# Kernel optimization log

Measured on AMD Instinct MI355X. Metric: run time of the kernel, lower is better.

## Reference

```python
import jax, jax.numpy as jnp
import numpy as np

FACTOR = 5

def setup_inputs() -> dict:
    key = jax.random.key(0)
    kq, kk, kv, ki = jax.random.split(key, 4)
    B, L, H, D = 8, 2048, 8, 64
    u = FACTOR * int(np.ceil(np.log(L)))  # sample_k == n_top == 40
    return {
        "queries": jax.random.normal(kq, (B, L, H, D), dtype=jnp.float32),
        "keys": jax.random.normal(kk, (B, L, H, D), dtype=jnp.float32),
        "values": jax.random.normal(kv, (B, L, H, D), dtype=jnp.float32),
        "index_sample": jax.random.randint(ki, (L, u), 0, L, dtype=jnp.int32),
    }

def reference(queries, keys, values, index_sample):
    B, L, H, D = queries.shape
    # faithful to torch .view(B, H, -1, D) on contiguous tensors (a reshape, not a transpose)
    q = queries.reshape(B, H, L, D)
    k = keys.reshape(B, H, L, D)
    v = values.reshape(B, H, L, D)
    u = FACTOR * int(np.ceil(np.log(L)))  # U_part == u
    # --- _prob_QK: sample keys per query, score, pick top-u queries ---
    K_sample = k[:, :, index_sample, :]                      # [B,H,L,u,D] gather over L_K
    QK_sample = jnp.einsum('bhld,bhlsd->bhls', q, K_sample)  # [B,H,L,u]
    M = QK_sample.max(axis=-1) - QK_sample.sum(axis=-1) / L  # sparsity measure [B,H,L]
    M_top = jax.lax.top_k(M, u)[1]                           # [B,H,u] indices of active queries
    Q_reduce = jnp.take_along_axis(q, M_top[..., None], axis=2)  # [B,H,u,D]
    scores = jnp.einsum('bhud,bhld->bhul', Q_reduce, k)      # [B,H,u,L]
    scale = 1.0 / float(np.sqrt(D))
    attn = jax.nn.softmax(scores * scale, axis=-1)           # dropout is identity in eval
    context = jnp.einsum('bhul,bhld->bhud', attn, v)         # [B,H,u,D]
    return context, attn
```

## Files before the change

kernel.cpp:

```cpp
#include <hip/hip_runtime.h>
#include <math.h>

#define LSEQ 2048
#define DDIM 64
#define UU   40
#define NBH  64
#define CTX_ELEMS (NBH*UU*DDIM)

__global__ __launch_bounds__(256, 4) void k12_sample_m(
    const float* __restrict__ q, const float* __restrict__ k,
    const int* __restrict__ idxs, float* __restrict__ M) {
  int b = blockIdx.x;
  int bh = b & 63;
  int ltile = b >> 6;
  int t = threadIdx.x;
  int g = t >> 2;
  int sub = t & 3;
  int l = ltile * 64 + g;

  const float4* qr = (const float4*)(q + (size_t)(bh * LSEQ + l) * DDIM);
  float4 qv[4];
#pragma unroll
  for (int m = 0; m < 4; ++m) qv[m] = qr[4 * m + sub];

  const float* kbase = k + (size_t)bh * LSEQ * DDIM;
  const int4* ir = (const int4*)(idxs + l * UU);

  float mx = -INFINITY, sm = 0.f;
#pragma unroll 1
  for (int s4 = 0; s4 < UU / 4; ++s4) {
    int4 jv = ir[s4];
    const float4* k0 = (const float4*)(kbase + (size_t)jv.x * DDIM);
    const float4* k1 = (const float4*)(kbase + (size_t)jv.y * DDIM);
    const float4* k2 = (const float4*)(kbase + (size_t)jv.z * DDIM);
    const float4* k3 = (const float4*)(kbase + (size_t)jv.w * DDIM);
    float d0 = 0.f, d1 = 0.f, d2 = 0.f, d3 = 0.f;
#pragma unroll
    for (int m = 0; m < 4; ++m) {
      float4 a = k0[4 * m + sub];
      float4 x = qv[m];
      d0 += x.x * a.x + x.y * a.y + x.z * a.z + x.w * a.w;
    }
#pragma unroll
    for (int m = 0; m < 4; ++m) {
      float4 a = k1[4 * m + sub];
      float4 x = qv[m];
      d1 += x.x * a.x + x.y * a.y + x.z * a.z + x.w * a.w;
    }
#pragma unroll
    for (int m = 0; m < 4; ++m) {
      float4 a = k2[4 * m + sub];
      float4 x = qv[m];
      d2 += x.x * a.x + x.y * a.y + x.z * a.z + x.w * a.w;
    }
#pragma unroll
    for (int m = 0; m < 4; ++m) {
      float4 a = k3[4 * m + sub];
      float4 x = qv[m];
      d3 += x.x * a.x + x.y * a.y + x.z * a.z + x.w * a.w;
    }
    d0 += __shfl_xor(d0, 1, 64); d0 += __shfl_xor(d0, 2, 64);
    d1 += __shfl_xor(d1, 1, 64); d1 += __shfl_xor(d1, 2, 64);
    d2 += __shfl_xor(d2, 1, 64); d2 += __shfl_xor(d2, 2, 64);
    d3 += __shfl_xor(d3, 1, 64); d3 += __shfl_xor(d3, 2, 64);
    mx = fmaxf(fmaxf(fmaxf(mx, d0), fmaxf(d1, d2)), d3);
    sm += (d0 + d1) + (d2 + d3);
  }
  if (sub == 0) M[bh * LSEQ + l] = mx - sm * (1.0f / (float)LSEQ);
}

__global__ __launch_bounds__(256) void k3_topk(const float* __restrict__ M,
                                               int* __restrict__ Mtop) {
  int bh = blockIdx.x;
  int t = threadIdx.x;
  int w = t >> 6;
  int lane = t & 63;
  float v[8];
#pragma unroll
  for (int j = 0; j < 8; ++j) v[j] = M[bh * LSEQ + t + 256 * j];
  __shared__ float swv[4];
  __shared__ int   swi[4];
  __shared__ int   win;
  for (int it = 0; it < UU; ++it) {
    float bv = -INFINITY; int bi = 0x7fffffff;
#pragma unroll
    for (int j = 0; j < 8; ++j) {
      if (v[j] > bv) { bv = v[j]; bi = t + 256 * j; }
    }
#pragma unroll
    for (int off = 32; off > 0; off >>= 1) {
      float ov = __shfl_xor(bv, off, 64);
      int   oi = __shfl_xor(bi, off, 64);
      if (ov > bv || (ov == bv && oi < bi)) { bv = ov; bi = oi; }
    }
    if (lane == 0) { swv[w] = bv; swi[w] = bi; }
    __syncthreads();
    if (t == 0) {
      float fv = swv[0]; int fi = swi[0];
#pragma unroll
      for (int j = 1; j < 4; ++j) {
        if (swv[j] > fv || (swv[j] == fv && swi[j] < fi)) { fv = swv[j]; fi = swi[j]; }
      }
      Mtop[bh * UU + it] = fi;
      win = fi;
    }
    __syncthreads();
    int wi = win;
    if ((wi & 255) == t) v[wi >> 8] = -INFINITY;
  }
}

__global__ __launch_bounds__(256, 4) void k45_scores_softmax(
    const float* __restrict__ q, const float* __restrict__ k,
    const int* __restrict__ Mtop, float* __restrict__ attn,
    float* __restrict__ ctx) {
  __shared__ float sct[4 * LSEQ];
  int b = blockIdx.x;
  int bh = b & 63;
  int u0 = (b >> 6) * 4;
  int t = threadIdx.x;
  int g = t >> 2;
  int sub = t & 3;

  ctx[b * 256 + t] = 0.f;

  float4 qv[4][4];
#pragma unroll
  for (int u = 0; u < 4; ++u) {
    int qi = Mtop[bh * UU + u0 + u];
    const float4* qr = (const float4*)(q + (size_t)(bh * LSEQ + qi) * DDIM);
#pragma unroll
    for (int m = 0; m < 4; ++m) qv[u][m] = qr[4 * m + sub];
  }

  const float* kb = k + (size_t)bh * LSEQ * DDIM;
#pragma unroll 1
  for (int p = 0; p < 32; ++p) {
    int l = p * 64 + g;
    const float4* kr = (const float4*)(kb + (size_t)l * DDIM);
    float4 ks[4];
#pragma unroll
    for (int m = 0; m < 4; ++m) ks[m] = kr[4 * m + sub];
    float d[4];
#pragma unroll
    for (int u = 0; u < 4; ++u) {
      float s = 0.f;
#pragma unroll
      for (int m = 0; m < 4; ++m) {
        float4 x = qv[u][m], a = ks[m];
        s += x.x * a.x + x.y * a.y + x.z * a.z + x.w * a.w;
      }
      s += __shfl_xor(s, 1, 64);
      s += __shfl_xor(s, 2, 64);
      d[u] = s * 0.125f;
    }
    if (sub == 0) {
#pragma unroll
      for (int u = 0; u < 4; ++u) sct[u * LSEQ + l] = d[u];
    }
  }
  __syncthreads();

  int w = t >> 6, lane = t & 63;
  float* row = sct + w * LSEQ;
  float vv[32];
  float mx = -INFINITY;
#pragma unroll
  for (int j = 0; j < 32; ++j) { vv[j] = row[lane + 64 * j]; mx = fmaxf(mx, vv[j]); }
#pragma unroll
  for (int off = 32; off > 0; off >>= 1) mx = fmaxf(mx, __shfl_xor(mx, off, 64));
  float sm = 0.f;
#pragma unroll
  for (int j = 0; j < 32; ++j) { vv[j] = __expf(vv[j] - mx); sm += vv[j]; }
#pragma unroll
  for (int off = 32; off > 0; off >>= 1) sm += __shfl_xor(sm, off, 64);
  float inv = 1.0f / sm;
  float* ap = attn + (size_t)(bh * UU + u0 + w) * LSEQ;
#pragma unroll
  for (int j = 0; j < 32; ++j) ap[lane + 64 * j] = vv[j] * inv;
}

__global__ __launch_bounds__(256) void k7_context(
    const float* __restrict__ attn, const float* __restrict__ v,
    float* __restrict__ ctx) {
  __shared__ float vt[256 * DDIM];
  int b = blockIdx.x;
  int bh = b & 63;
  int l0 = (b >> 6) * 256;
  int t = threadIdx.x;

  const float4* src = (const float4*)(v + ((size_t)bh * LSEQ + l0) * DDIM);
  float4* dst = (float4*)vt;
#pragma unroll
  for (int i = 0; i < 16; ++i) dst[t + 256 * i] = src[t + 256 * i];
  __syncthreads();

  int w = t >> 6;
  int d = t & 63;
  const float* ab = attn + ((size_t)bh * UU + w * 10) * LSEQ + l0;
  float acc[10];
#pragma unroll
  for (int u = 0; u < 10; ++u) acc[u] = 0.f;
#pragma unroll 1
  for (int l4 = 0; l4 < 64; ++l4) {
    int l = l4 * 4;
    float4 av[10];
#pragma unroll
    for (int u = 0; u < 10; ++u)
      av[u] = *(const float4*)(ab + (size_t)u * LSEQ + l);
#pragma unroll
    for (int i = 0; i < 4; ++i) {
      float vvv = vt[(l + i) * DDIM + d];
#pragma unroll
      for (int u = 0; u < 10; ++u)
        acc[u] = fmaf(((const float*)&av[u])[i], vvv, acc[u]);
    }
  }
#pragma unroll
  for (int u = 0; u < 10; ++u)
    atomicAdd(&ctx[((size_t)bh * UU + w * 10 + u) * DDIM + d], acc[u]);
}

extern "C" void kernel_launch(void* const* d_in, const int* in_sizes, int n_in,
                              void* d_out, int out_size, void* d_ws, size_t ws_size,
                              hipStream_t stream) {
  const float* q   = (const float*)d_in[0];
  const float* k   = (const float*)d_in[1];
  const float* v   = (const float*)d_in[2];
  const int*   idx = (const int*)d_in[3];

  float* ctx  = (float*)d_out;
  float* attn = (float*)d_out + CTX_ELEMS;

  float* M    = (float*)d_ws;
  int*   Mtop = (int*)(M + NBH * LSEQ);

  k12_sample_m<<<NBH * 32, 256, 0, stream>>>(q, k, idx, M);
  k3_topk<<<NBH, 256, 0, stream>>>(M, Mtop);
  k45_scores_softmax<<<NBH * 10, 256, 0, stream>>>(q, k, Mtop, attn, ctx);
  k7_context<<<NBH * 8, 256, 0, stream>>>(attn, v, ctx);
}
```

Baseline: 303.9 us.

## Fuse top-k, scores/softmax and context into one kernel per head group

Merges the top-k selection, score/softmax and attention-times-V kernels into a single kernel with 8 blocks per head, each handling 5 selected queries. Every block redundantly recomputes the full 40-step top-k from M so that no Mtop round trip or separate launch is needed. The context product now reads normalized probabilities from shared memory instead of re-reading attn from global, and reduces across warps in shared memory instead of using atomics and a zero-init pass. The cost is 8x redundant top-k work, fewer blocks for the score phase (512 vs 640), and more shared memory per block.

Measured after the change: 327.5 us. +7.8%, slower.

```diff
diff --git a/kernel.cpp b/kernel.cpp
--- a/kernel.cpp
+++ b/kernel.cpp
@@ -37,26 +37,22 @@
     float d0 = 0.f, d1 = 0.f, d2 = 0.f, d3 = 0.f;
 #pragma unroll
     for (int m = 0; m < 4; ++m) {
-      float4 a = k0[4 * m + sub];
-      float4 x = qv[m];
+      float4 a = k0[4 * m + sub]; float4 x = qv[m];
       d0 += x.x * a.x + x.y * a.y + x.z * a.z + x.w * a.w;
     }
 #pragma unroll
     for (int m = 0; m < 4; ++m) {
-      float4 a = k1[4 * m + sub];
-      float4 x = qv[m];
+      float4 a = k1[4 * m + sub]; float4 x = qv[m];
       d1 += x.x * a.x + x.y * a.y + x.z * a.z + x.w * a.w;
     }
 #pragma unroll
     for (int m = 0; m < 4; ++m) {
-      float4 a = k2[4 * m + sub];
-      float4 x = qv[m];
+      float4 a = k2[4 * m + sub]; float4 x = qv[m];
       d2 += x.x * a.x + x.y * a.y + x.z * a.z + x.w * a.w;
     }
 #pragma unroll
     for (int m = 0; m < 4; ++m) {
-      float4 a = k3[4 * m + sub];
-      float4 x = qv[m];
+      float4 a = k3[4 * m + sub]; float4 x = qv[m];
       d3 += x.x * a.x + x.y * a.y + x.z * a.z + x.w * a.w;
     }
     d0 += __shfl_xor(d0, 1, 64); d0 += __shfl_xor(d0, 2, 64);
@@ -69,23 +65,32 @@
   if (sub == 0) M[bh * LSEQ + l] = mx - sm * (1.0f / (float)LSEQ);
 }
 
-__global__ __launch_bounds__(256) void k3_topk(const float* __restrict__ M,
-                                               int* __restrict__ Mtop) {
-  int bh = blockIdx.x;
-  int t = threadIdx.x;
-  int w = t >> 6;
-  int lane = t & 63;
-  float v[8];
-#pragma unroll
-  for (int j = 0; j < 8; ++j) v[j] = M[bh * LSEQ + t + 256 * j];
+__global__ __launch_bounds__(256, 3) void kf_fused(
+    const float* __restrict__ q, const float* __restrict__ k,
+    const float* __restrict__ v, const float* __restrict__ M,
+    float* __restrict__ attn, float* __restrict__ ctx) {
+  __shared__ float sct[5 * LSEQ];
+  __shared__ float red[4 * 5 * 64];
   __shared__ float swv[4];
   __shared__ int   swi[4];
   __shared__ int   win;
+  __shared__ int   topq[5];
+
+  int b = blockIdx.x;
+  int bh = b & 63;
+  int ug = b >> 6;
+  int u0 = ug * 5;
+  int t = threadIdx.x;
+  int w = t >> 6, lane = t & 63;
+
+  float mv[8];
+#pragma unroll
+  for (int j = 0; j < 8; ++j) mv[j] = M[bh * LSEQ + t + 256 * j];
   for (int it = 0; it < UU; ++it) {
     float bv = -INFINITY; int bi = 0x7fffffff;
 #pragma unroll
     for (int j = 0; j < 8; ++j) {
-      if (v[j] > bv) { bv = v[j]; bi = t + 256 * j; }
+      if (mv[j] > bv) { bv = mv[j]; bi = t + 256 * j; }
     }
 #pragma unroll
     for (int off = 32; off > 0; off >>= 1) {
@@ -101,38 +106,24 @@
       for (int j = 1; j < 4; ++j) {
         if (swv[j] > fv || (swv[j] == fv && swi[j] < fi)) { fv = swv[j]; fi = swi[j]; }
       }
-      Mtop[bh * UU + it] = fi;
       win = fi;
+      if (it >= u0 && it < u0 + 5) topq[it - u0] = fi;
     }
     __syncthreads();
     int wi = win;
-    if ((wi & 255) == t) v[wi >> 8] = -INFINITY;
-  }
-}
-
-__global__ __launch_bounds__(256, 4) void k45_scores_softmax(
-    const float* __restrict__ q, const float* __restrict__ k,
-    const int* __restrict__ Mtop, float* __restrict__ attn,
-    float* __restrict__ ctx) {
-  __shared__ float sct[4 * LSEQ];
-  int b = blockIdx.x;
-  int bh = b & 63;
-  int u0 = (b >> 6) * 4;
-  int t = threadIdx.x;
+    if ((wi & 255) == t) mv[wi >> 8] = -INFINITY;
+  }
+
   int g = t >> 2;
   int sub = t & 3;
-
-  ctx[b * 256 + t] = 0.f;
-
-  float4 qv[4][4];
-#pragma unroll
-  for (int u = 0; u < 4; ++u) {
-    int qi = Mtop[bh * UU + u0 + u];
+  float4 qv[5][4];
+#pragma unroll
+  for (int u = 0; u < 5; ++u) {
+    int qi = topq[u];
     const float4* qr = (const float4*)(q + (size_t)(bh * LSEQ + qi) * DDIM);
 #pragma unroll
     for (int m = 0; m < 4; ++m) qv[u][m] = qr[4 * m + sub];
   }
-
   const float* kb = k + (size_t)bh * LSEQ * DDIM;
 #pragma unroll 1
   for (int p = 0; p < 32; ++p) {
@@ -141,9 +132,8 @@
     float4 ks[4];
 #pragma unroll
     for (int m = 0; m < 4; ++m) ks[m] = kr[4 * m + sub];
-    float d[4];
-#pragma unroll
-    for (int u = 0; u < 4; ++u) {
+#pragma unroll
+    for (int u = 0; u < 5; ++u) {
       float s = 0.f;
 #pragma unroll
       for (int m = 0; m < 4; ++m) {
@@ -152,73 +142,68 @@
       }
       s += __shfl_xor(s, 1, 64);
       s += __shfl_xor(s, 2, 64);
-      d[u] = s * 0.125f;
-    }
-    if (sub == 0) {
-#pragma unroll
-      for (int u = 0; u < 4; ++u) sct[u * LSEQ + l] = d[u];
+      if (sub == 0) sct[u * LSEQ + l] = s * 0.125f;
     }
   }
   __syncthreads();
 
-  int w = t >> 6, lane = t & 63;
-  float* row = sct + w * LSEQ;
-  float vv[32];
-  float mx = -INFINITY;
-#pragma unroll
-  for (int j = 0; j < 32; ++j) { vv[j] = row[lane + 64 * j]; mx = fmaxf(mx, vv[j]); }
-#pragma unroll
-  for (int off = 32; off > 0; off >>= 1) mx = fmaxf(mx, __shfl_xor(mx, off, 64));
-  float sm = 0.f;
-#pragma unroll
-  for (int j = 0; j < 32; ++j) { vv[j] = __expf(vv[j] - mx); sm += vv[j]; }
-#pragma unroll
-  for (int off = 32; off > 0; off >>= 1) sm += __shfl_xor(sm, off, 64);
-  float inv = 1.0f / sm;
-  float* ap = attn + (size_t)(bh * UU + u0 + w) * LSEQ;
-#pragma unroll
-  for (int j = 0; j < 32; ++j) ap[lane + 64 * j] = vv[j] * inv;
-}
-
-__global__ __launch_bounds__(256) void k7_context(
-    const float* __restrict__ attn, const float* __restrict__ v,
-    float* __restrict__ ctx) {
-  __shared__ float vt[256 * DDIM];
-  int b = blockIdx.x;
-  int bh = b & 63;
-  int l0 = (b >> 6) * 256;
-  int t = threadIdx.x;
-
-  const float4* src = (const float4*)(v + ((size_t)bh * LSEQ + l0) * DDIM);
-  float4* dst = (float4*)vt;
-#pragma unroll
-  for (int i = 0; i < 16; ++i) dst[t + 256 * i] = src[t + 256 * i];
+  for (int r = w; r < 5; r += 4) {
+    float* row = sct + r * LSEQ;
+    float vv[32];
+    float mx = -INFINITY;
+#pragma unroll
+    for (int j = 0; j < 32; ++j) { vv[j] = row[lane + 64 * j]; mx = fmaxf(mx, vv[j]); }
+#pragma unroll
+    for (int off = 32; off > 0; off >>= 1) mx = fmaxf(mx, __shfl_xor(mx, off, 64));
+    float sm = 0.f;
+#pragma unroll
+    for (int j = 0; j < 32; ++j) { vv[j] = __expf(vv[j] - mx); sm += vv[j]; }
+#pragma unroll
+    for (int off = 32; off > 0; off >>= 1) sm += __shfl_xor(sm, off, 64);
+    float inv = 1.0f / sm;
+    float* ap = attn + (size_t)(bh * UU + u0 + r) * LSEQ;
+#pragma unroll
+    for (int j = 0; j < 32; ++j) {
+      float pn = vv[j] * inv;
+      ap[lane + 64 * j] = pn;
+      row[lane + 64 * j] = pn;
+    }
+  }
   __syncthreads();
 
-  int w = t >> 6;
-  int d = t & 63;
-  const float* ab = attn + ((size_t)bh * UU + w * 10) * LSEQ + l0;
-  float acc[10];
-#pragma unroll
-  for (int u = 0; u < 10; ++u) acc[u] = 0.f;
+  int d = lane;
+  const float* vb = v + (size_t)bh * LSEQ * DDIM;
+  float acc[5] = {0.f, 0.f, 0.f, 0.f, 0.f};
+  int l0 = w * 512;
 #pragma unroll 1
-  for (int l4 = 0; l4 < 64; ++l4) {
-    int l = l4 * 4;
-    float4 av[10];
-#pragma unroll
-    for (int u = 0; u < 10; ++u)
-      av[u] = *(const float4*)(ab + (size_t)u * LSEQ + l);
-#pragma unroll
-    for (int i = 0; i < 4; ++i) {
-      float vvv = vt[(l + i) * DDIM + d];
-#pragma unroll
-      for (int u = 0; u < 10; ++u)
-        acc[u] = fmaf(((const float*)&av[u])[i], vvv, acc[u]);
-    }
-  }
-#pragma unroll
-  for (int u = 0; u < 10; ++u)
-    atomicAdd(&ctx[((size_t)bh * UU + w * 10 + u) * DDIM + d], acc[u]);
+  for (int i = 0; i < 128; ++i) {
+    int l = l0 + i * 4;
+    float4 p0 = *(float4*)&sct[0 * LSEQ + l];
+    float4 p1 = *(float4*)&sct[1 * LSEQ + l];
+    float4 p2 = *(float4*)&sct[2 * LSEQ + l];
+    float4 p3 = *(float4*)&sct[3 * LSEQ + l];
+    float4 p4 = *(float4*)&sct[4 * LSEQ + l];
+    float v0 = vb[(size_t)(l + 0) * DDIM + d];
+    float v1 = vb[(size_t)(l + 1) * DDIM + d];
+    float v2 = vb[(size_t)(l + 2) * DDIM + d];
+    float v3 = vb[(size_t)(l + 3) * DDIM + d];
+    acc[0] = fmaf(p0.x, v0, fmaf(p0.y, v1, fmaf(p0.z, v2, fmaf(p0.w, v3, acc[0]))));
+    acc[1] = fmaf(p1.x, v0, fmaf(p1.y, v1, fmaf(p1.z, v2, fmaf(p1.w, v3, acc[1]))));
+    acc[2] = fmaf(p2.x, v0, fmaf(p2.y, v1, fmaf(p2.z, v2, fmaf(p2.w, v3, acc[2]))));
+    acc[3] = fmaf(p3.x, v0, fmaf(p3.y, v1, fmaf(p3.z, v2, fmaf(p3.w, v3, acc[3]))));
+    acc[4] = fmaf(p4.x, v0, fmaf(p4.y, v1, fmaf(p4.z, v2, fmaf(p4.w, v3, acc[4]))));
+  }
+#pragma unroll
+  for (int u = 0; u < 5; ++u) red[(w * 5 + u) * 64 + d] = acc[u];
+  __syncthreads();
+  if (w == 0) {
+#pragma unroll
+    for (int u = 0; u < 5; ++u) {
+      float s = red[(0 * 5 + u) * 64 + d] + red[(1 * 5 + u) * 64 + d] +
+                red[(2 * 5 + u) * 64 + d] + red[(3 * 5 + u) * 64 + d];
+      ctx[(size_t)(bh * UU + u0 + u) * DDIM + d] = s;
+    }
+  }
 }
 
 extern "C" void kernel_launch(void* const* d_in, const int* in_sizes, int n_in,
@@ -233,10 +218,7 @@
   float* attn = (float*)d_out + CTX_ELEMS;
 
   float* M    = (float*)d_ws;
-  int*   Mtop = (int*)(M + NBH * LSEQ);
 
   k12_sample_m<<<NBH * 32, 256, 0, stream>>>(q, k, idx, M);
-  k3_topk<<<NBH, 256, 0, stream>>>(M, Mtop);
-  k45_scores_softmax<<<NBH * 10, 256, 0, stream>>>(q, k, Mtop, attn, ctx);
-  k7_context<<<NBH * 8, 256, 0, stream>>>(attn, v, ctx);
+  kf_fused<<<NBH * 8, 256, 0, stream>>>(q, k, v, M, attn, ctx);
 }
```
